# Kernel tuning notes

Measured on AMD Instinct MI355X. Metric: run time of the kernel, lower is better.

Reference implementation:

```python
import jax, jax.numpy as jnp
import numpy as np

H = 12          # num heads
D = 128         # head dim
C = 1536        # hidden size (= H*D)
L = 4           # encoder blocks
I = 4096        # gated-MLP intermediate
M = 6144        # merger hidden
PD = 1176       # flattened patch dim
S = 1600        # num patches (40x40 grid)
G = 40          # max grid size
EPS = 1e-6
ROPE_THETA = 10000.0


def setup_inputs() -> dict:
    key = jax.random.key(0)
    ks = jax.random.split(key, 24)
    w = lambda k, shape: jax.random.normal(k, shape, jnp.float32) * 0.02
    inp = {
        'pixel_values': jax.random.normal(ks[0], (S, PD), jnp.float32),
        'pos_ids': jax.random.randint(ks[1], (S, 2), 0, G),
        'max_grid_size': G,
        'w_patch': w(ks[2], (PD, C)),
        # per-block stacked params (scanned over leading L axis)
        'qkv_w': w(ks[3], (L, C, 3 * C)),
        'qkv_b': jnp.zeros((L, 3 * C), jnp.float32),
        'q_norm_w': jnp.ones((L, D), jnp.float32),
        'k_norm_w': jnp.ones((L, D), jnp.float32),
        'proj_w': w(ks[4], (L, C, C)),
        'proj_b': jnp.zeros((L, C), jnp.float32),
        'norm1_w': jnp.ones((L, C), jnp.float32),
        'norm2_w': jnp.ones((L, C), jnp.float32),
        'gate_w': w(ks[5], (L, C, I)),
        'up_w': w(ks[6], (L, C, I)),
        'down_w': w(ks[7], (L, I, C)),
        # post / downsample / merger
        'post_ln_w': jnp.ones((C,), jnp.float32),
        'conv_w': w(ks[8], (C, C, 2, 2)),   # Conv2d(C->C, k=2, s=2)
        'conv_b': jnp.zeros((C,), jnp.float32),
        'fc1_w': w(ks[9], (C, M)),
        'fc1_b': jnp.zeros((M,), jnp.float32),
        'fc2_w': w(ks[10], (M, C)),
        'fc2_b': jnp.zeros((C,), jnp.float32),
    }
    return inp


def _rmsnorm(x, w):
    v = jnp.mean(jnp.square(x.astype(jnp.float32)), axis=-1, keepdims=True)
    return (x.astype(jnp.float32) * jax.lax.rsqrt(v + EPS)).astype(x.dtype) * w


def _rotate_half(x):
    x1, x2 = jnp.split(x, 2, axis=-1)
    return jnp.concatenate([-x2, x1], axis=-1)


def reference(pixel_values, pos_ids, max_grid_size, w_patch, qkv_w, qkv_b,
              q_norm_w, k_norm_w, proj_w, proj_b, norm1_w, norm2_w,
              gate_w, up_w, down_w, post_ln_w, conv_w, conv_b,
              fc1_w, fc1_b, fc2_w, fc2_b):
    seq = pixel_values.shape[0]
    scale = D ** -0.5

    # --- rotary table: rot dim per head = D//2, inv_freq len D//4 ---
    rdim = D // 2
    inv_freq = 1.0 / (ROPE_THETA ** (jnp.arange(0, rdim, 2, dtype=jnp.float32) / rdim))
    freqs = jnp.arange(max_grid_size, dtype=jnp.float32)[:, None] * inv_freq  # [G, D//4]
    rope = freqs[pos_ids].reshape(seq, -1)        # [S, D//2] (h,w interleaved)
    emb = jnp.concatenate([rope, rope], axis=-1)  # [S, D]
    cos = jnp.cos(emb)[:, None, :]                # [S, 1, D] broadcast over heads
    sin = jnp.sin(emb)[:, None, :]

    h = pixel_values @ w_patch  # patch embed (Conv3d == linear on flattened patch)

    def block(h, p):
        (qw, qb, qn, kn, pw, pb, n1, n2, gw, uw, dw) = p
        x = _rmsnorm(h, n1)
        qkv = (x @ qw + qb).reshape(seq, 3, H, D)
        q, k, v = qkv[:, 0], qkv[:, 1], qkv[:, 2]   # [S, H, D]
        q = _rmsnorm(q, qn)
        k = _rmsnorm(k, kn)
        q = q * cos + _rotate_half(q) * sin
        k = k * cos + _rotate_half(k) * sin
        scores = jnp.einsum('shd,thd->hst', q, k) * scale          # [H, S, S]
        attn = jax.nn.softmax(scores.astype(jnp.float32), axis=-1).astype(q.dtype)
        o = jnp.einsum('hst,thd->shd', attn, v).reshape(seq, H * D)
        h = h + o @ pw + pb
        x2 = _rmsnorm(h, n2)
        h = h + (jax.nn.silu(x2 @ gw) * (x2 @ uw)) @ dw
        return h, None

    h, _ = jax.lax.scan(block, h, (qkv_w, qkv_b, q_norm_w, k_norm_w, proj_w,
                                   proj_b, norm1_w, norm2_w, gate_w, up_w, down_w))

    h = _rmsnorm(h, post_ln_w)
    # 2x2 spatial merge via strided conv: [S/4, C, 2, 2] -> [S/4, C]
    h4 = h.reshape(-1, 2, 2, C).transpose(0, 3, 1, 2)
    d = jnp.einsum('ncij,ocij->no', h4, conv_w) + conv_b
    out = jax.nn.gelu(d @ fc1_w + fc1_b) @ fc2_w + fc2_b
    return out
```

## Files before the change

kernel.cpp:

```cpp
#include <hip/hip_runtime.h>
#include <math.h>

typedef __bf16 bf16_t;
typedef float f32x4 __attribute__((ext_vector_type(4)));
typedef __bf16 bf16x8 __attribute__((ext_vector_type(8)));

union FragU { uint4 u; bf16x8 b; };

#define MFMA_BF16(a, b, c) __builtin_amdgcn_mfma_f32_16x16x32_bf16((a), (b), (c), 0, 0, 0)

__device__ __forceinline__ void glds16(const void* g, void* l) {
  __builtin_amdgcn_global_load_lds((const __attribute__((address_space(1))) void*)g,
                                   (__attribute__((address_space(3))) void*)l, 16, 0, 0);
}

__global__ void rope_k(const int* __restrict__ pos_ids, float* __restrict__ cosb,
                       float* __restrict__ sinb) {
  int s = blockIdx.x;
  int d = threadIdx.x;
  int pair = d >> 5, j = d & 31;
  float p = (float)pos_ids[s * 2 + pair];
  float inv = powf(10000.f, -(float)j / 32.f);
  float v = p * inv;
  float c = cosf(v), sn = sinf(v);
  cosb[s * 128 + d] = c;  cosb[s * 128 + d + 64] = c;
  sinb[s * 128 + d] = sn; sinb[s * 128 + d + 64] = sn;
}

__global__ __launch_bounds__(256) void rmsnorm_bf_k(const float* __restrict__ in,
                                                    const float* __restrict__ w,
                                                    bf16_t* __restrict__ out, int cols) {
  int row = blockIdx.x;
  const float* x = in + (size_t)row * cols;
  float ss = 0.f;
  for (int c = threadIdx.x; c < cols; c += 256) { float v = x[c]; ss = fmaf(v, v, ss); }
#pragma unroll
  for (int o = 32; o; o >>= 1) ss += __shfl_xor(ss, o);
  __shared__ float red[4];
  if ((threadIdx.x & 63) == 0) red[threadIdx.x >> 6] = ss;
  __syncthreads();
  float tot = red[0] + red[1] + red[2] + red[3];
  float rs = rsqrtf(tot / (float)cols + 1e-6f);
  bf16_t* y = out + (size_t)row * cols;
  for (int c = threadIdx.x; c < cols; c += 256) y[c] = (bf16_t)(x[c] * rs * w[c]);
}

__global__ __launch_bounds__(256) void transpose_cvt_k(const float* __restrict__ in,
                                                       bf16_t* __restrict__ out,
                                                       int K, int N, int Kpad) {
  __shared__ float t[32][33];
  int k0 = blockIdx.x * 32, n0 = blockIdx.y * 32;
  int tx = threadIdx.x & 31, ty = threadIdx.x >> 5;
#pragma unroll
  for (int i = 0; i < 4; ++i) {
    int k = k0 + ty + 8 * i;
    t[ty + 8 * i][tx] = (k < K) ? in[(size_t)k * N + n0 + tx] : 0.f;
  }
  __syncthreads();
#pragma unroll
  for (int i = 0; i < 4; ++i) {
    int n = n0 + ty + 8 * i;
    out[(size_t)n * Kpad + k0 + tx] = (bf16_t)t[tx][ty + 8 * i];
  }
}

__global__ void convert_pad_k(const float* __restrict__ in, bf16_t* __restrict__ out,
                              int R, int K, int Kpad) {
  int idx = blockIdx.x * 256 + threadIdx.x;
  if (idx < R * Kpad) {
    int r = idx / Kpad, k = idx - r * Kpad;
    out[idx] = (k < K) ? (bf16_t)in[(size_t)r * K + k] : (bf16_t)0.f;
  }
}

__global__ __launch_bounds__(128) void qknorm_rope_k(const bf16_t* __restrict__ qkv,
    const float* __restrict__ qn, const float* __restrict__ kn,
    const float* __restrict__ cosb, const float* __restrict__ sinb,
    bf16_t* __restrict__ qo, bf16_t* __restrict__ ko) {
  const int s = blockIdx.x / 12, h = blockIdx.x % 12;
  const int d = threadIdx.x;
  __shared__ float nrm[128];
  __shared__ float red[2];
  const float cs = cosb[s * 128 + d], sn = sinb[s * 128 + d];
  const float QS = 0.08838834764831845f * 1.4426950408889634f;
#pragma unroll
  for (int part = 0; part < 2; ++part) {
    const bf16_t* p = qkv + (size_t)s * 4608 + part * 1536 + h * 128;
    float v = (float)p[d];
    float ss = v * v;
#pragma unroll
    for (int o = 32; o; o >>= 1) ss += __shfl_xor(ss, o);
    if ((d & 63) == 0) red[d >> 6] = ss;
    __syncthreads();
    float rs = rsqrtf((red[0] + red[1]) * (1.f / 128.f) + 1e-6f);
    float nv = v * rs * (part ? kn[d] : qn[d]);
    nrm[d] = nv;
    __syncthreads();
    float rot = (d < 64) ? -nrm[d + 64] : nrm[d - 64];
    float val = nv * cs + rot * sn;
    bf16_t* dst = part ? ko : qo;
    dst[((size_t)h * 1600 + s) * 128 + d] = (bf16_t)(part ? val : val * QS);
    __syncthreads();
  }
}

__global__ __launch_bounds__(256) void vtrans_k(const bf16_t* __restrict__ qkv,
                                                bf16_t* __restrict__ vt) {
  __shared__ __align__(16) bf16_t t[128][136];
  const int h = blockIdx.x, s0 = blockIdx.y * 128;
  const int tx = threadIdx.x & 15, ty = threadIdx.x >> 4;
#pragma unroll
  for (int i = 0; i < 8; ++i) {
    int sl = ty + 16 * i, s = s0 + sl;
    uint4 v = {0u, 0u, 0u, 0u};
    if (s < 1600) v = *(const uint4*)&qkv[(size_t)s * 4608 + 3072 + h * 128 + tx * 8];
    *(uint4*)&t[sl][tx * 8] = v;
  }
  __syncthreads();
  if (s0 + tx * 8 < 1600) {
#pragma unroll
    for (int i = 0; i < 8; ++i) {
      int dd = ty + 16 * i;
      bf16_t tmp[8];
#pragma unroll
      for (int j = 0; j < 8; ++j) tmp[j] = t[tx * 8 + j][dd];
      *(uint4*)&vt[(size_t)(h * 128 + dd) * 1600 + s0 + tx * 8] = *(uint4*)tmp;
    }
  }
}

__global__ __launch_bounds__(256) void attn_mfma(const bf16_t* __restrict__ qg,
    const bf16_t* __restrict__ kg, const bf16_t* __restrict__ vg,
    bf16_t* __restrict__ o) {
  const int bid = blockIdx.x;
  const int xcd = bid & 7, sub = bid >> 3;
  const int swz = (xcd < 4 ? xcd * 38 : 4 * 38 + (xcd - 4) * 37) + sub;
  const int h = swz / 25;
  const int q0 = (swz % 25) * 64;
  const int tid = threadIdx.x;
  const int w = tid >> 6, lane = tid & 63;
  const int fq = lane >> 4, fr = lane & 15;
  const bf16_t* qh = qg + (size_t)h * 1600 * 128;
  const bf16_t* kh = kg + (size_t)h * 1600 * 128;
  const bf16_t* vh = vg + (size_t)h * 128 * 1600;
  __shared__ __align__(16) bf16_t Ks[3][4096];
  __shared__ __align__(16) bf16_t Vs[3][4096];
  __shared__ __align__(16) bf16_t pl[4][512];
  int off_k[2], off_v[2], ldsb[2];
#pragma unroll
  for (int c = 0; c < 2; ++c) {
    int j = c * 256 + tid;
    off_k[c] = (j & 31) * 128 + (j >> 5) * 8;
    off_v[c] = (j & 127) * 1600 + (j >> 7) * 8;
    ldsb[c] = (c * 256 + w * 64) * 8;
  }
  FragU aq[4];
#pragma unroll
  for (int db = 0; db < 4; ++db)
    aq[db].u = *(const uint4*)&qh[(size_t)(q0 + w * 16 + fr) * 128 + db * 32 + fq * 8];
  f32x4 zero = {0.f, 0.f, 0.f, 0.f};
  f32x4 oacc[8];
#pragma unroll
  for (int nb = 0; nb < 8; ++nb) oacc[nb] = zero;
  float lrun[4] = {0.f, 0.f, 0.f, 0.f};
#pragma unroll
  for (int c = 0; c < 2; ++c) {
    glds16(kh + off_k[c], &Ks[0][ldsb[c]]);
    glds16(vh + off_v[c], &Vs[0][ldsb[c]]);
  }
#pragma unroll
  for (int c = 0; c < 2; ++c) {
    glds16(kh + 32 * 128 + off_k[c], &Ks[1][ldsb[c]]);
    glds16(vh + 32 + off_v[c], &Vs[1][ldsb[c]]);
  }
  asm volatile("s_waitcnt vmcnt(4)" ::: "memory");
  __builtin_amdgcn_s_barrier();
  int cur = 0;
  for (int t = 0; t < 50; ++t) {
    int stg = cur + 2; if (stg >= 3) stg -= 3;
    if (t + 2 < 50) {
      const int kb = (t + 2) * 32;
#pragma unroll
      for (int c = 0; c < 2; ++c) {
        glds16(kh + (size_t)kb * 128 + off_k[c], &Ks[stg][ldsb[c]]);
        glds16(vh + kb + off_v[c], &Vs[stg][ldsb[c]]);
      }
    }
    f32x4 s0 = zero, s1 = zero;
#pragma unroll
    for (int db = 0; db < 4; ++db) {
      FragU bk0, bk1;
      bk0.u = *(const uint4*)&Ks[cur][((db * 4 + fq) * 32 + fr) * 8];
      bk1.u = *(const uint4*)&Ks[cur][((db * 4 + fq) * 32 + 16 + fr) * 8];
      s0 = MFMA_BF16(aq[db].b, bk0.b, s0);
      s1 = MFMA_BF16(aq[db].b, bk1.b, s1);
    }
    float p0[4], p1[4];
#pragma unroll
    for (int r = 0; r < 4; ++r) {
      p0[r] = exp2f(s0[r] - 16.f);
      p1[r] = exp2f(s1[r] - 16.f);
      lrun[r] += p0[r] + p1[r];
    }
#pragma unroll
    for (int r = 0; r < 4; ++r) {
      int q = fq * 4 + r;
      int kk0 = fr;
      pl[w][((kk0 >> 3) * 16 + q) * 8 + (kk0 & 7)] = (bf16_t)p0[r];
      int kk1 = 16 + fr;
      pl[w][((kk1 >> 3) * 16 + q) * 8 + (kk1 & 7)] = (bf16_t)p1[r];
    }
    FragU ap;
    ap.u = *(const uint4*)&pl[w][(fq * 16 + fr) * 8];
#pragma unroll
    for (int nb = 0; nb < 8; ++nb) {
      FragU bv;
      bv.u = *(const uint4*)&Vs[cur][(fq * 128 + nb * 16 + fr) * 8];
      oacc[nb] = MFMA_BF16(ap.b, bv.b, oacc[nb]);
    }
    if (t + 2 < 50) asm volatile("s_waitcnt vmcnt(4)" ::: "memory");
    else            asm volatile("s_waitcnt vmcnt(0)" ::: "memory");
    __builtin_amdgcn_s_barrier();
    cur = cur + 1; if (cur == 3) cur = 0;
  }
#pragma unroll
  for (int r = 0; r < 4; ++r) {
    lrun[r] += __shfl_xor(lrun[r], 1);
    lrun[r] += __shfl_xor(lrun[r], 2);
    lrun[r] += __shfl_xor(lrun[r], 4);
    lrun[r] += __shfl_xor(lrun[r], 8);
  }
  float inv_[4];
#pragma unroll
  for (int r = 0; r < 4; ++r) inv_[r] = 1.f / lrun[r];
#pragma unroll
  for (int nb = 0; nb < 8; ++nb)
#pragma unroll
    for (int r = 0; r < 4; ++r) {
      int qq = q0 + w * 16 + fq * 4 + r;
      o[(size_t)qq * 1536 + h * 128 + nb * 16 + fr] = (bf16_t)(oacc[nb][r] * inv_[r]);
    }
}

__global__ void silu_mul_k(bf16_t* __restrict__ gu) {
  int i = blockIdx.x * 256 + threadIdx.x;
  if (i < 1600 * 1024) {
    int m = i >> 10, j = (i & 1023) * 4;
    size_t base = (size_t)m * 8192 + j;
    union U { uint2 v; bf16_t b[4]; };
    U gv, uv, ov;
    gv.v = *(const uint2*)&gu[base];
    uv.v = *(const uint2*)&gu[base + 4096];
#pragma unroll
    for (int jj = 0; jj < 4; ++jj) {
      float x = (float)gv.b[jj], y = (float)uv.b[jj];
      ov.b[jj] = (bf16_t)(x / (1.f + __expf(-x)) * y);
    }
    *(uint2*)&gu[base] = ov.v;
  }
}

__global__ void gather_conv_k(const bf16_t* __restrict__ hf, bf16_t* __restrict__ abuf) {
  int idx = blockIdx.x * 256 + threadIdx.x;
  if (idx < 400 * 6144) {
    int n = idx / 6144, k = idx - n * 6144;
    abuf[idx] = hf[(size_t)(4 * n + (k & 3)) * 1536 + (k >> 2)];
  }
}

template <int ACT, int BIAS, int RES, int OBF>
__global__ __launch_bounds__(256) void gemm64(const bf16_t* __restrict__ A,
    const bf16_t* __restrict__ Bt, const float* __restrict__ bias,
    const float* __restrict__ res, float* __restrict__ outf,
    bf16_t* __restrict__ outb, int M, int N, int K, int lda) {
  __shared__ __align__(16) bf16_t As[3][2048];
  __shared__ __align__(16) bf16_t Bs[3][2048];
  const int tid = threadIdx.x;
  const int lane = tid & 63, w = tid >> 6;
  const int m0 = blockIdx.y * 64, n0 = blockIdx.x * 64;
  const int fq = lane >> 4, fr = lane & 15;
  const int wc = w * 16;
  const bf16_t* ag = A + (size_t)(m0 + lane) * lda + w * 8;
  const bf16_t* bg = Bt + (size_t)(n0 + lane) * K + w * 8;
  f32x4 zero = {0.f, 0.f, 0.f, 0.f};
  f32x4 acc[4];
#pragma unroll
  for (int m = 0; m < 4; ++m) acc[m] = zero;
  const int nt = K >> 5;
  glds16(ag, &As[0][w * 512]); glds16(bg, &Bs[0][w * 512]);
  ag += 32; bg += 32;
  glds16(ag, &As[1][w * 512]); glds16(bg, &Bs[1][w * 512]);
  ag += 32; bg += 32;
  asm volatile("s_waitcnt vmcnt(2)" ::: "memory");
  __builtin_amdgcn_s_barrier();
  int cur = 0;
  for (int t = 0; t < nt; ++t) {
    int stg = cur + 2; if (stg >= 3) stg -= 3;
    if (t + 2 < nt) {
      glds16(ag, &As[stg][w * 512]); glds16(bg, &Bs[stg][w * 512]);
      ag += 32; bg += 32;
    }
    FragU bw, af[4];
    bw.u = *(const uint4*)&Bs[cur][(fq * 64 + wc + fr) * 8];
#pragma unroll
    for (int m = 0; m < 4; ++m)
      af[m].u = *(const uint4*)&As[cur][(fq * 64 + m * 16 + fr) * 8];
#pragma unroll
    for (int m = 0; m < 4; ++m)
      acc[m] = MFMA_BF16(af[m].b, bw.b, acc[m]);
    if (t + 2 < nt) asm volatile("s_waitcnt vmcnt(2)" ::: "memory");
    else            asm volatile("s_waitcnt vmcnt(0)" ::: "memory");
    __builtin_amdgcn_s_barrier();
    cur = cur + 1; if (cur == 3) cur = 0;
  }
#pragma unroll
  for (int m = 0; m < 4; ++m) {
#pragma unroll
    for (int r = 0; r < 4; ++r) {
      int gm = m0 + m * 16 + fq * 4 + r;
      if (gm < M) {
        int gn = n0 + wc + fr;
        float v = acc[m][r];
        if (BIAS) v += bias[gn];
        if (ACT == 1) {
          float x = v;
          float t = 0.7978845608028654f * fmaf(0.044715f * x, x * x, x);
          float e = exp2f(t * 2.8853900817779268f);
          v = x * e / (e + 1.f);
        }
        if (RES) v += res[(size_t)gm * N + gn];
        if (OBF) outb[(size_t)gm * N + gn] = (bf16_t)v;
        else outf[(size_t)gm * N + gn] = v;
      }
    }
  }
}

template <int ACT, int BIAS, int RES, int OBF>
__global__ __launch_bounds__(256) void gemm128(const bf16_t* __restrict__ A,
    const bf16_t* __restrict__ Bt, const float* __restrict__ bias,
    const float* __restrict__ res, float* __restrict__ outf,
    bf16_t* __restrict__ outb, int M, int N, int K, int lda) {
  __shared__ __align__(16) bf16_t As[3][4096];
  __shared__ __align__(16) bf16_t Bs[3][4096];
  const int tid = threadIdx.x;
  const int lane = tid & 63, w = tid >> 6;
  const int m0 = blockIdx.y * 128, n0 = blockIdx.x * 128;
  const int wr = (w >> 1) * 64, wc = (w & 1) * 64;
  const int fq = lane >> 4, fr = lane & 15;
  const int u1 = w * 64 + lane, u2 = u1 + 256;
  const int r1 = u1 & 127, c1 = u1 >> 7;
  const int r2 = u2 & 127, c2 = u2 >> 7;
  const bf16_t* a1 = A + (size_t)(m0 + r1) * lda + c1 * 8;
  const bf16_t* a2 = A + (size_t)(m0 + r2) * lda + c2 * 8;
  const bf16_t* b1 = Bt + (size_t)(n0 + r1) * K + c1 * 8;
  const bf16_t* b2 = Bt + (size_t)(n0 + r2) * K + c2 * 8;
  f32x4 zero = {0.f, 0.f, 0.f, 0.f};
  f32x4 acc[4][4];
#pragma unroll
  for (int m = 0; m < 4; ++m)
#pragma unroll
    for (int n = 0; n < 4; ++n) acc[m][n] = zero;
  const int nt = K >> 5;
  glds16(a1, &As[0][w * 512]); glds16(a2, &As[0][2048 + w * 512]);
  glds16(b1, &Bs[0][w * 512]); glds16(b2, &Bs[0][2048 + w * 512]);
  a1 += 32; a2 += 32; b1 += 32; b2 += 32;
  glds16(a1, &As[1][w * 512]); glds16(a2, &As[1][2048 + w * 512]);
  glds16(b1, &Bs[1][w * 512]); glds16(b2, &Bs[1][2048 + w * 512]);
  a1 += 32; a2 += 32; b1 += 32; b2 += 32;
  asm volatile("s_waitcnt vmcnt(4)" ::: "memory");
  __builtin_amdgcn_s_barrier();
  int cur = 0;
  for (int t = 0; t < nt; ++t) {
    int stg = cur + 2; if (stg >= 3) stg -= 3;
    if (t + 2 < nt) {
      glds16(a1, &As[stg][w * 512]); glds16(a2, &As[stg][2048 + w * 512]);
      glds16(b1, &Bs[stg][w * 512]); glds16(b2, &Bs[stg][2048 + w * 512]);
      a1 += 32; a2 += 32; b1 += 32; b2 += 32;
    }
    FragU af[4], bw[4];
#pragma unroll
    for (int m = 0; m < 4; ++m)
      af[m].u = *(const uint4*)&As[cur][(fq * 128 + wr + m * 16 + fr) * 8];
#pragma unroll
    for (int n = 0; n < 4; ++n)
      bw[n].u = *(const uint4*)&Bs[cur][(fq * 128 + wc + n * 16 + fr) * 8];
#pragma unroll
    for (int m = 0; m < 4; ++m)
#pragma unroll
      for (int n = 0; n < 4; ++n)
        acc[m][n] = MFMA_BF16(af[m].b, bw[n].b, acc[m][n]);
    if (t + 2 < nt) asm volatile("s_waitcnt vmcnt(4)" ::: "memory");
    else            asm volatile("s_waitcnt vmcnt(0)" ::: "memory");
    __builtin_amdgcn_s_barrier();
    cur = cur + 1; if (cur == 3) cur = 0;
  }
#pragma unroll
  for (int m = 0; m < 4; ++m) {
#pragma unroll
    for (int r = 0; r < 4; ++r) {
      int gm = m0 + wr + m * 16 + fq * 4 + r;
      if (gm < M) {
#pragma unroll
        for (int n = 0; n < 4; ++n) {
          int gn = n0 + wc + n * 16 + fr;
          float v = acc[m][n][r];
          if (BIAS) v += bias[gn];
          if (ACT == 1) {
            float x = v;
            float t2 = 0.7978845608028654f * fmaf(0.044715f * x, x * x, x);
            float e = exp2f(t2 * 2.8853900817779268f);
            v = x * e / (e + 1.f);
          }
          if (RES) v += res[(size_t)gm * N + gn];
          if (OBF) outb[(size_t)gm * N + gn] = (bf16_t)v;
          else outf[(size_t)gm * N + gn] = v;
        }
      }
    }
  }
}

__global__ __launch_bounds__(512, 2) void gemm256sq(const bf16_t* __restrict__ A,
    const bf16_t* __restrict__ Bt, bf16_t* __restrict__ outb,
    int M, int N, int K, int lda) {
  __shared__ __align__(16) bf16_t As[3][8192];
  __shared__ __align__(16) bf16_t Bs[3][8192];
  const int tid = threadIdx.x;
  const int lane = tid & 63, w = tid >> 6;
  const int m0 = blockIdx.y * 256, n0 = blockIdx.x * 256;
  const int wr = (w >> 2) * 128, wc = (w & 3) * 64;
  const int fq = lane >> 4, fr = lane & 15;
  const int f0 = tid, f1 = 512 + tid;
  const int r0 = f0 & 255, c0 = f0 >> 8;
  const int r1 = f1 & 255, c1 = f1 >> 8;
  const bf16_t* a0 = A + (size_t)(m0 + r0) * lda + c0 * 8;
  const bf16_t* a1 = A + (size_t)(m0 + r1) * lda + c1 * 8;
  const bf16_t* b0 = Bt + (size_t)(n0 + r0) * K + c0 * 8;
  const bf16_t* b1 = Bt + (size_t)(n0 + r1) * K + c1 * 8;
  const int l0 = (w * 64) * 8;
  const int l1 = (512 + w * 64) * 8;
  f32x4 zero = {0.f, 0.f, 0.f, 0.f};
  f32x4 acc[8][4];
#pragma unroll
  for (int m = 0; m < 8; ++m)
#pragma unroll
    for (int n = 0; n < 4; ++n) acc[m][n] = zero;
  const int nt = K >> 5;
  glds16(a0, &As[0][l0]); glds16(a1, &As[0][l1]);
  glds16(b0, &Bs[0][l0]); glds16(b1, &Bs[0][l1]);
  a0 += 32; a1 += 32; b0 += 32; b1 += 32;
  glds16(a0, &As[1][l0]); glds16(a1, &As[1][l1]);
  glds16(b0, &Bs[1][l0]); glds16(b1, &Bs[1][l1]);
  a0 += 32; a1 += 32; b0 += 32; b1 += 32;
  asm volatile("s_waitcnt vmcnt(4)" ::: "memory");
  __builtin_amdgcn_s_barrier();
  int cur = 0;
  for (int t = 0; t < nt; ++t) {
    int stg = cur + 2; if (stg >= 3) stg -= 3;
    if (t + 2 < nt) {
      glds16(a0, &As[stg][l0]); glds16(a1, &As[stg][l1]);
      glds16(b0, &Bs[stg][l0]); glds16(b1, &Bs[stg][l1]);
      a0 += 32; a1 += 32; b0 += 32; b1 += 32;
    }
    FragU bw[4];
#pragma unroll
    for (int n = 0; n < 4; ++n)
      bw[n].u = *(const uint4*)&Bs[cur][(fq * 256 + wc + n * 16 + fr) * 8];
    __builtin_amdgcn_s_setprio(1);
#pragma unroll
    for (int m = 0; m < 8; ++m) {
      FragU af;
      af.u = *(const uint4*)&As[cur][(fq * 256 + wr + m * 16 + fr) * 8];
#pragma unroll
      for (int n = 0; n < 4; ++n)
        acc[m][n] = MFMA_BF16(af.b, bw[n].b, acc[m][n]);
    }
    __builtin_amdgcn_s_setprio(0);
    if (t + 2 < nt) asm volatile("s_waitcnt vmcnt(4)" ::: "memory");
    else            asm volatile("s_waitcnt vmcnt(0)" ::: "memory");
    __builtin_amdgcn_s_barrier();
    cur = cur + 1; if (cur == 3) cur = 0;
  }
#pragma unroll
  for (int m = 0; m < 8; ++m) {
#pragma unroll
    for (int r = 0; r < 4; ++r) {
      int gm = m0 + wr + m * 16 + fq * 4 + r;
      if (gm < M) {
#pragma unroll
        for (int n = 0; n < 4; ++n) {
          int gn = n0 + wc + n * 16 + fr;
          outb[(size_t)gm * N + gn] = (bf16_t)acc[m][n][r];
        }
      }
    }
  }
}

extern "C" void kernel_launch(void* const* d_in, const int* in_sizes, int n_in,
                              void* d_out, int out_size, void* d_ws, size_t ws_size,
                              hipStream_t stream) {
  (void)in_sizes; (void)n_in; (void)out_size; (void)ws_size;
  const float* pixel     = (const float*)d_in[0];
  const int*   pos_ids   = (const int*)d_in[1];
  const float* w_patch   = (const float*)d_in[3];
  const float* qkv_w     = (const float*)d_in[4];
  const float* qkv_b     = (const float*)d_in[5];
  const float* q_norm_w  = (const float*)d_in[6];
  const float* k_norm_w  = (const float*)d_in[7];
  const float* proj_w    = (const float*)d_in[8];
  const float* proj_b    = (const float*)d_in[9];
  const float* norm1_w   = (const float*)d_in[10];
  const float* norm2_w   = (const float*)d_in[11];
  const float* gate_w    = (const float*)d_in[12];
  const float* up_w      = (const float*)d_in[13];
  const float* down_w    = (const float*)d_in[14];
  const float* post_ln_w = (const float*)d_in[15];
  const float* conv_w    = (const float*)d_in[16];
  const float* conv_b    = (const float*)d_in[17];
  const float* fc1_w     = (const float*)d_in[18];
  const float* fc1_b     = (const float*)d_in[19];
  const float* fc2_w     = (const float*)d_in[20];
  const float* fc2_b     = (const float*)d_in[21];
  float* out = (float*)d_out;

  char* wsb = (char*)d_ws;
  float*  h     = (float*)(wsb + 0);
  bf16_t* xo    = (bf16_t*)(wsb + 9830400);
  char*   R1    = wsb + 14745600;
  bf16_t* qkvb  = (bf16_t*)(R1);
  bf16_t* qb    = (bf16_t*)(R1 + 14745600);
  bf16_t* kb    = (bf16_t*)(R1 + 19660800);
  bf16_t* vb    = (bf16_t*)(R1 + 24576000);
  bf16_t* gub   = (bf16_t*)(R1);
  bf16_t* pixb  = (bf16_t*)(R1);
  bf16_t* ab    = (bf16_t*)(R1);
  bf16_t* dbuf  = (bf16_t*)(R1 + 4915200);
  bf16_t* ebuf  = (bf16_t*)(R1 + 6144000);
  float*  cosb  = (float*)(wsb + 44236800);
  float*  sinb  = (float*)(wsb + 45056000);
  char*   W     = wsb + 45875200;
  bf16_t* qkvwT = (bf16_t*)(W);
  bf16_t* projT = (bf16_t*)(W + 14155776);
  bf16_t* gateupT = (bf16_t*)(W + 18874368);
  bf16_t* upT   = (bf16_t*)(W + 31457280);
  bf16_t* downT = (bf16_t*)(W + 44040192);
  bf16_t* convB = (bf16_t*)(W);
  bf16_t* fc1T  = (bf16_t*)(W + 18874368);
  bf16_t* fc2T  = (bf16_t*)(W + 37748736);
  bf16_t* wpT   = (bf16_t*)(wsb + 102498304);

  rope_k<<<1600, 64, 0, stream>>>(pos_ids, cosb, sinb);
  convert_pad_k<<<(1600 * 1184 + 255) / 256, 256, 0, stream>>>(pixel, pixb, 1600, 1176, 1184);
  transpose_cvt_k<<<dim3(37, 48), 256, 0, stream>>>(w_patch, wpT, 1176, 1536, 1184);
  gemm64<0, 0, 0, 0><<<dim3(24, 25), 256, 0, stream>>>(
      pixb, wpT, nullptr, nullptr, h, nullptr, 1600, 1536, 1184, 1184);

  for (int l = 0; l < 4; ++l) {
    const float* qw = qkv_w  + (size_t)l * 1536 * 4608;
    const float* pw = proj_w + (size_t)l * 1536 * 1536;
    const float* gw = gate_w + (size_t)l * 1536 * 4096;
    const float* uw = up_w   + (size_t)l * 1536 * 4096;
    const float* dw = down_w + (size_t)l * 4096 * 1536;
    transpose_cvt_k<<<dim3(48, 144), 256, 0, stream>>>(qw, qkvwT, 1536, 4608, 1536);
    transpose_cvt_k<<<dim3(48, 48),  256, 0, stream>>>(pw, projT, 1536, 1536, 1536);
    transpose_cvt_k<<<dim3(48, 128), 256, 0, stream>>>(gw, gateupT, 1536, 4096, 1536);
    transpose_cvt_k<<<dim3(48, 128), 256, 0, stream>>>(uw, upT,   1536, 4096, 1536);
    transpose_cvt_k<<<dim3(128, 48), 256, 0, stream>>>(dw, downT, 4096, 1536, 4096);

    rmsnorm_bf_k<<<1600, 256, 0, stream>>>(h, norm1_w + (size_t)l * 1536, xo, 1536);
    gemm128<0, 1, 0, 1><<<dim3(36, 13), 256, 0, stream>>>(
        xo, qkvwT, qkv_b + (size_t)l * 4608, nullptr, nullptr, qkvb, 1600, 4608, 1536, 1536);
    qknorm_rope_k<<<1600 * 12, 128, 0, stream>>>(
        qkvb, q_norm_w + (size_t)l * 128, k_norm_w + (size_t)l * 128, cosb, sinb, qb, kb);
    vtrans_k<<<dim3(12, 13), 256, 0, stream>>>(qkvb, vb);
    attn_mfma<<<300, 256, 0, stream>>>(qb, kb, vb, xo);
    gemm64<0, 1, 1, 0><<<dim3(24, 25), 256, 0, stream>>>(
        xo, projT, proj_b + (size_t)l * 1536, h, h, nullptr, 1600, 1536, 1536, 1536);
    rmsnorm_bf_k<<<1600, 256, 0, stream>>>(h, norm2_w + (size_t)l * 1536, xo, 1536);
    gemm256sq<<<dim3(32, 7), 512, 0, stream>>>(
        xo, gateupT, gub, 1600, 8192, 1536, 1536);
    silu_mul_k<<<6400, 256, 0, stream>>>(gub);
    gemm64<0, 0, 1, 0><<<dim3(24, 25), 256, 0, stream>>>(
        gub, downT, nullptr, h, h, nullptr, 1600, 1536, 4096, 8192);
  }

  convert_pad_k<<<(1536 * 6144 + 255) / 256, 256, 0, stream>>>(conv_w, convB, 1536, 6144, 6144);
  transpose_cvt_k<<<dim3(48, 192), 256, 0, stream>>>(fc1_w, fc1T, 1536, 6144, 1536);
  transpose_cvt_k<<<dim3(192, 48), 256, 0, stream>>>(fc2_w, fc2T, 6144, 1536, 6144);
  rmsnorm_bf_k<<<1600, 256, 0, stream>>>(h, post_ln_w, xo, 1536);
  gather_conv_k<<<(400 * 6144 + 255) / 256, 256, 0, stream>>>(xo, ab);
  gemm64<0, 1, 0, 1><<<dim3(24, 7), 256, 0, stream>>>(
      ab, convB, conv_b, nullptr, nullptr, dbuf, 400, 1536, 6144, 6144);
  gemm64<1, 1, 0, 1><<<dim3(96, 7), 256, 0, stream>>>(
      dbuf, fc1T, fc1_b, nullptr, nullptr, ebuf, 400, 6144, 1536, 1536);
  gemm64<0, 1, 0, 0><<<dim3(24, 7), 256, 0, stream>>>(
      ebuf, fc2T, fc2_b, nullptr, out, nullptr, 400, 1536, 6144, 6144);
}
```

Measured before the change: 2.250 ms.

## Split-K the merger conv and fc2 GEMMs to fill the GPU

```diff
diff --git a/kernel.cpp b/kernel.cpp
--- a/kernel.cpp
+++ b/kernel.cpp
@@ -333,6 +333,88 @@
         else outf[(size_t)gm * N + gn] = v;
       }
     }
+  }
+}
+
+template <int KS>
+__global__ __launch_bounds__(256) void gemm64sk(const bf16_t* __restrict__ A,
+    const bf16_t* __restrict__ Bt, float* __restrict__ part,
+    int M, int N, int K, int lda) {
+  __shared__ __align__(16) bf16_t As[3][2048];
+  __shared__ __align__(16) bf16_t Bs[3][2048];
+  const int tid = threadIdx.x;
+  const int lane = tid & 63, w = tid >> 6;
+  const int m0 = blockIdx.y * 64, n0 = blockIdx.x * 64;
+  const int fq = lane >> 4, fr = lane & 15;
+  const int wc = w * 16;
+  const int kchunk = K / KS;
+  const int kbase = blockIdx.z * kchunk;
+  const bf16_t* ag = A + (size_t)(m0 + lane) * lda + kbase + w * 8;
+  const bf16_t* bg = Bt + (size_t)(n0 + lane) * K + kbase + w * 8;
+  f32x4 zero = {0.f, 0.f, 0.f, 0.f};
+  f32x4 acc[4];
+#pragma unroll
+  for (int m = 0; m < 4; ++m) acc[m] = zero;
+  const int nt = kchunk >> 5;
+  glds16(ag, &As[0][w * 512]); glds16(bg, &Bs[0][w * 512]);
+  ag += 32; bg += 32;
+  glds16(ag, &As[1][w * 512]); glds16(bg, &Bs[1][w * 512]);
+  ag += 32; bg += 32;
+  asm volatile("s_waitcnt vmcnt(2)" ::: "memory");
+  __builtin_amdgcn_s_barrier();
+  int cur = 0;
+  for (int t = 0; t < nt; ++t) {
+    int stg = cur + 2; if (stg >= 3) stg -= 3;
+    if (t + 2 < nt) {
+      glds16(ag, &As[stg][w * 512]); glds16(bg, &Bs[stg][w * 512]);
+      ag += 32; bg += 32;
+    }
+    FragU bw, af[4];
+    bw.u = *(const uint4*)&Bs[cur][(fq * 64 + wc + fr) * 8];
+#pragma unroll
+    for (int m = 0; m < 4; ++m)
+      af[m].u = *(const uint4*)&As[cur][(fq * 64 + m * 16 + fr) * 8];
+#pragma unroll
+    for (int m = 0; m < 4; ++m)
+      acc[m] = MFMA_BF16(af[m].b, bw.b, acc[m]);
+    if (t + 2 < nt) asm volatile("s_waitcnt vmcnt(2)" ::: "memory");
+    else            asm volatile("s_waitcnt vmcnt(0)" ::: "memory");
+    __builtin_amdgcn_s_barrier();
+    cur = cur + 1; if (cur == 3) cur = 0;
+  }
+  float* ps = part + (size_t)blockIdx.z * M * N;
+#pragma unroll
+  for (int m = 0; m < 4; ++m) {
+#pragma unroll
+    for (int r = 0; r < 4; ++r) {
+      int gm = m0 + m * 16 + fq * 4 + r;
+      if (gm < M) {
+        int gn = n0 + wc + fr;
+        ps[(size_t)gm * N + gn] = acc[m][r];
+      }
+    }
+  }
+}
+
+template <int KS, int ACT, int OBF>
+__global__ void reduce_sk(const float* __restrict__ part, const float* __restrict__ bias,
+                          float* __restrict__ outf, bf16_t* __restrict__ outb,
+                          int M, int N) {
+  int idx = blockIdx.x * 256 + threadIdx.x;
+  if (idx < M * N) {
+    int n = idx % N;
+    float v = 0.f;
+#pragma unroll
+    for (int s = 0; s < KS; ++s) v += part[(size_t)s * M * N + idx];
+    v += bias[n];
+    if (ACT == 1) {
+      float x = v;
+      float t = 0.7978845608028654f * fmaf(0.044715f * x, x * x, x);
+      float e = exp2f(t * 2.8853900817779268f);
+      v = x * e / (e + 1.f);
+    }
+    if (OBF) outb[idx] = (bf16_t)v;
+    else outf[idx] = v;
   }
 }
 
@@ -538,6 +620,7 @@
   bf16_t* ab    = (bf16_t*)(R1);
   bf16_t* dbuf  = (bf16_t*)(R1 + 4915200);
   bf16_t* ebuf  = (bf16_t*)(R1 + 6144000);
+  float*  skp   = (float*)(R1 + 11059200);
   float*  cosb  = (float*)(wsb + 44236800);
   float*  sinb  = (float*)(wsb + 45056000);
   char*   W     = wsb + 45875200;
@@ -591,10 +674,12 @@
   transpose_cvt_k<<<dim3(192, 48), 256, 0, stream>>>(fc2_w, fc2T, 6144, 1536, 6144);
   rmsnorm_bf_k<<<1600, 256, 0, stream>>>(h, post_ln_w, xo, 1536);
   gather_conv_k<<<(400 * 6144 + 255) / 256, 256, 0, stream>>>(xo, ab);
-  gemm64<0, 1, 0, 1><<<dim3(24, 7), 256, 0, stream>>>(
-      ab, convB, conv_b, nullptr, nullptr, dbuf, 400, 1536, 6144, 6144);
+  gemm64sk<4><<<dim3(24, 7, 4), 256, 0, stream>>>(ab, convB, skp, 400, 1536, 6144, 6144);
+  reduce_sk<4, 0, 1><<<(400 * 1536 + 255) / 256, 256, 0, stream>>>(
+      skp, conv_b, nullptr, dbuf, 400, 1536);
   gemm64<1, 1, 0, 1><<<dim3(96, 7), 256, 0, stream>>>(
       dbuf, fc1T, fc1_b, nullptr, nullptr, ebuf, 400, 6144, 1536, 1536);
-  gemm64<0, 1, 0, 0><<<dim3(24, 7), 256, 0, stream>>>(
-      ebuf, fc2T, fc2_b, nullptr, out, nullptr, 400, 1536, 6144, 6144);
-}
+  gemm64sk<4><<<dim3(24, 7, 4), 256, 0, stream>>>(ebuf, fc2T, skp, 400, 1536, 6144, 6144);
+  reduce_sk<4, 0, 0><<<(400 * 1536 + 255) / 256, 256, 0, stream>>>(
+      skp, fc2_b, out, nullptr, 400, 1536);
+}
```

New measurement: 2.111 ms. 6.2% less time.
